# Kernel optimization log

Measured on AMD Instinct MI355X. Metric: run time of the kernel, lower is better.

Reference implementation:

```python
import jax, jax.numpy as jnp
import numpy as np

N, B, I = 64, 32, 1
EMBED, ACT, DETER, STOCH, HIDDEN = 1536, 16, 2048, 512, 1024
EPS = 1e-5


def _ln(x, g, b):
    m = jnp.mean(x, -1, keepdims=True)
    v = jnp.mean((x - m) ** 2, -1, keepdims=True)
    return (x - m) / jnp.sqrt(v + EPS) * g + b


def setup_inputs() -> dict:
    key = jax.random.key(0)
    ks = jax.random.split(key, 24)
    s = 0.02
    d = {
        "embed": jax.random.normal(ks[0], (N, B, EMBED), jnp.float32),
        "action": jax.random.normal(ks[1], (N, B, ACT), jnp.float32),
        "reset": jnp.zeros((N, B), jnp.bool_),
        "h0": jnp.zeros((B * I, DETER), jnp.float32),
        "z0": jnp.zeros((B * I, STOCH), jnp.float32),
        "noises": jax.random.normal(ks[2], (N, B, I, STOCH), jnp.float32),
        # params
        "W_z": jax.random.normal(ks[3], (HIDDEN, STOCH)) * s,
        "b_z": jnp.zeros((HIDDEN,)),
        "W_a": jax.random.normal(ks[4], (HIDDEN, ACT)) * s,
        "ln_in_g": jnp.ones((HIDDEN,)), "ln_in_b": jnp.zeros((HIDDEN,)),
        "gru_Wih": jax.random.normal(ks[5], (3 * DETER, HIDDEN)) * s,
        "gru_Whh": jax.random.normal(ks[6], (3 * DETER, DETER)) * s,
        "gru_bih": jnp.zeros((3 * DETER,)), "gru_bhh": jnp.zeros((3 * DETER,)),
        "W_ph": jax.random.normal(ks[7], (HIDDEN, DETER)) * s,
        "b_ph": jnp.zeros((HIDDEN,)),
        "W_pe": jax.random.normal(ks[8], (HIDDEN, EMBED)) * s,
        "ln_post_g": jnp.ones((HIDDEN,)), "ln_post_b": jnp.zeros((HIDDEN,)),
        "W_post": jax.random.normal(ks[9], (2 * STOCH, HIDDEN)) * s,
        "b_post": jnp.zeros((2 * STOCH,)),
        "W_prh": jax.random.normal(ks[10], (HIDDEN, DETER)) * s,
        "b_prh": jnp.zeros((HIDDEN,)),
        "ln_pr_g": jnp.ones((HIDDEN,)), "ln_pr_b": jnp.zeros((HIDDEN,)),
        "W_pr": jax.random.normal(ks[11], (2 * STOCH, HIDDEN)) * s,
        "b_pr": jnp.zeros((2 * STOCH,)),
    }
    return d


def _core(embed, action, reset, h0, z0, noises,
          W_z, b_z, W_a, ln_in_g, ln_in_b,
          gru_Wih, gru_Whh, gru_bih, gru_bhh,
          W_ph, b_ph, W_pe, ln_post_g, ln_post_b, W_post, b_post,
          W_prh, b_prh, ln_pr_g, ln_pr_b, W_pr, b_pr):
    n, b = embed.shape[:2]
    # expand to (n, b*I, .) ; I == 1
    embeds = embed.reshape(n, b * I, -1)
    actions = action.reshape(n, b * I, -1)
    masks = (~reset).astype(jnp.float32).reshape(n, b * I, 1)
    noise = noises.reshape(n, b * I, -1)

    def step(carry, xs):
        h, z = carry
        e_t, a_t, m_t, n_t = xs
        h = h * m_t
        z = z * m_t
        x = z @ W_z.T + b_z + a_t @ W_a.T
        za = jax.nn.elu(_ln(x, ln_in_g, ln_in_b))
        # torch GRUCell
        gi = za @ gru_Wih.T + gru_bih
        gh = h @ gru_Whh.T + gru_bhh
        gi_r, gi_u, gi_n = jnp.split(gi, 3, -1)
        gh_r, gh_u, gh_n = jnp.split(gh, 3, -1)
        r = jax.nn.sigmoid(gi_r + gh_r)
        u = jax.nn.sigmoid(gi_u + gh_u)
        cand = jnp.tanh(gi_n + r * gh_n)
        h_new = (1.0 - u) * cand + u * h
        x = h_new @ W_ph.T + b_ph + e_t @ W_pe.T
        post_in = jax.nn.elu(_ln(x, ln_post_g, ln_post_b))
        post = post_in @ W_post.T + b_post
        mean, std_raw = jnp.split(post, 2, -1)
        std = jax.nn.softplus(std_raw) + 0.1
        sample = mean + std * n_t
        return (h_new, sample), (post, h_new, sample)

    (h_last, z_last), (posts, states_h, samples) = jax.lax.scan(
        step, (h0, z0), (embeds, actions, masks, noise))

    # batch prior over all h
    x = states_h @ W_prh.T + b_prh
    x = jax.nn.elu(_ln(x, ln_pr_g, ln_pr_b))
    priors = x @ W_pr.T + b_pr
    features = jnp.concatenate([states_h, samples], -1)

    rs = lambda t: t.reshape(n, b, I, -1)
    return rs(priors), rs(posts), rs(samples), rs(features), h_last, z_last


def reference(embed, action, reset, h0, z0, noises,
              W_z, b_z, W_a, ln_in_g, ln_in_b,
              gru_Wih, gru_Whh, gru_bih, gru_bhh,
              W_ph, b_ph, W_pe, ln_post_g, ln_post_b, W_post, b_post,
              W_prh, b_prh, ln_pr_g, ln_pr_b, W_pr, b_pr):
    return _core(embed, action, reset, h0, z0, noises,
                 W_z, b_z, W_a, ln_in_g, ln_in_b,
                 gru_Wih, gru_Whh, gru_bih, gru_bhh,
                 W_ph, b_ph, W_pe, ln_post_g, ln_post_b, W_post, b_post,
                 W_prh, b_prh, ln_pr_g, ln_pr_b, W_pr, b_pr)
```

## Files before the change

kernel.cpp:

```cpp
#include <hip/hip_runtime.h>
#include <hip/hip_bf16.h>
#include <stdint.h>

#define NSTEP 64
#define BATCH 32
#define EMBED_D 1536
#define ACT_D 16
#define DETER 2048
#define STOCH 512
#define HIDDEN 1024
#define FEAT 2560
#define NBLK 256

typedef __attribute__((ext_vector_type(8))) short bf16x8;
typedef __attribute__((ext_vector_type(4))) float f32x4;

#define MFMA16 __builtin_amdgcn_mfma_f32_16x16x32_bf16
#define AGENT __HIP_MEMORY_SCOPE_AGENT

__device__ __forceinline__ float eluf(float x) { return x > 0.f ? x : expf(x) - 1.f; }
__device__ __forceinline__ float sigf(float x) { return 1.f / (1.f + expf(-x)); }
__device__ __forceinline__ unsigned short f2bf(float f) {
    __hip_bfloat16 h = __float2bfloat16(f);
    return __builtin_bit_cast(unsigned short, h);
}
__device__ __forceinline__ float bf2f(unsigned short u) {
    unsigned v = ((unsigned)u) << 16;
    return __builtin_bit_cast(float, v);
}

__device__ __forceinline__ void stc_u32(unsigned* p, unsigned v) {
    __hip_atomic_store(p, v, __ATOMIC_RELAXED, AGENT);
}
__device__ __forceinline__ void stc_u64(unsigned long long* p, unsigned long long v) {
    __hip_atomic_store(p, v, __ATOMIC_RELAXED, AGENT);
}
__device__ __forceinline__ unsigned long long ldc_u64(const unsigned long long* p) {
    return __hip_atomic_load(p, __ATOMIC_RELAXED, AGENT);
}
__device__ __forceinline__ float ldc_f32(const float* p) {
    return __hip_atomic_load(p, __ATOMIC_RELAXED, AGENT);
}
__device__ __forceinline__ int ldc_i32(const int* p) {
    return __hip_atomic_load(p, __ATOMIC_RELAXED, AGENT);
}
__device__ __forceinline__ void stc_i32(int* p, int v) {
    __hip_atomic_store(p, v, __ATOMIC_RELAXED, AGENT);
}
__device__ __forceinline__ bf16x8 ldc_bf8(const unsigned short* p) {
    union { unsigned long long q[2]; bf16x8 v; } u;
    u.q[0] = ldc_u64((const unsigned long long*)p);
    u.q[1] = ldc_u64((const unsigned long long*)(p + 4));
    return u.v;
}
__device__ __forceinline__ ushort4 ldc_us4(const unsigned short* p) {
    unsigned long long q = ldc_u64((const unsigned long long*)p);
    return __builtin_bit_cast(ushort4, q);
}

__device__ __forceinline__ void gbar3(int* flags, int* release, int epoch) {
    asm volatile("s_waitcnt vmcnt(0)" ::: "memory");
    __syncthreads();
    if (blockIdx.x == 0) {
        int tid = threadIdx.x;
        if (tid >= 1 && tid < NBLK) {
            while (ldc_i32(&flags[tid * 32]) < epoch) __builtin_amdgcn_s_sleep(4);
        }
        asm volatile("" ::: "memory");
        __syncthreads();
        if (tid < 32) stc_i32(&release[tid * 32], epoch);
    } else {
        if (threadIdx.x == 0) {
            stc_i32(&flags[blockIdx.x * 32], epoch);
            int* rel = &release[(blockIdx.x & 31) * 32];
            while (ldc_i32(rel) < epoch) __builtin_amdgcn_s_sleep(4);
        }
        asm volatile("" ::: "memory");
        __syncthreads();
    }
}

__global__ __launch_bounds__(256) void k_cvt_all(
    const float* __restrict__ s0, unsigned short* __restrict__ d0,
    const float* __restrict__ s1, unsigned short* __restrict__ d1,
    const float* __restrict__ s2, unsigned short* __restrict__ d2,
    const float* __restrict__ s3, unsigned short* __restrict__ d3,
    const float* __restrict__ s4, unsigned short* __restrict__ d4)
{
    long long e = ((long long)blockIdx.x * 256 + threadIdx.x) * 4;
    const float* src; unsigned short* dst; long long off;
    if (e < 524288)        { src = s0; dst = d0; off = e; }
    else if (e < 6815744)  { src = s1; dst = d1; off = e - 524288; }
    else if (e < 19398656) { src = s2; dst = d2; off = e - 6815744; }
    else if (e < 21495808) { src = s3; dst = d3; off = e - 19398656; }
    else if (e < 22544384) { src = s4; dst = d4; off = e - 21495808; }
    else return;
    float4 v = *reinterpret_cast<const float4*>(src + off);
    ushort4 o;
    o.x = f2bf(v.x); o.y = f2bf(v.y); o.z = f2bf(v.z); o.w = f2bf(v.w);
    *reinterpret_cast<ushort4*>(dst + off) = o;
}

__global__ __launch_bounds__(256) void k_setup(
    const float* __restrict__ h0, const float* __restrict__ z0,
    const uint8_t* __restrict__ reset0,
    float* __restrict__ h0m, unsigned short* __restrict__ h16m0,
    unsigned short* __restrict__ z16m, int* __restrict__ flags)
{
    int gid = blockIdx.x * 256 + threadIdx.x;
    int idx = gid * 4;
    if (idx < BATCH * DETER) {
        int b = idx >> 11;
        float m = reset0[b] ? 0.f : 1.f;
        float4 v = *reinterpret_cast<const float4*>(h0 + idx);
        v.x *= m; v.y *= m; v.z *= m; v.w *= m;
        *reinterpret_cast<float4*>(h0m + idx) = v;
        ushort4 o;
        o.x = f2bf(v.x); o.y = f2bf(v.y); o.z = f2bf(v.z); o.w = f2bf(v.w);
        *reinterpret_cast<ushort4*>(h16m0 + idx) = o;
    } else if (idx < BATCH * DETER + BATCH * STOCH) {
        int zi = idx - BATCH * DETER;
        int b = zi >> 9;
        float m = reset0[b] ? 0.f : 1.f;
        float4 v = *reinterpret_cast<const float4*>(z0 + zi);
        ushort4 o;
        o.x = f2bf(v.x * m); o.y = f2bf(v.y * m); o.z = f2bf(v.z * m); o.w = f2bf(v.w * m);
        *reinterpret_cast<ushort4*>(z16m + zi) = o;
    }
    if (gid < 9216) flags[gid] = 0;
}

__global__ __launch_bounds__(256) void k_preA(
    const float* __restrict__ action, const float* __restrict__ Wa,
    const float* __restrict__ bz, float* __restrict__ preA)
{
    __shared__ float al[16];
    int r = blockIdx.x, t = threadIdx.x;
    if (t < 16) al[t] = action[r * 16 + t];
    __syncthreads();
#pragma unroll
    for (int c = 0; c < 4; ++c) {
        int j = t + c * 256;
        const float* wr = Wa + j * 16;
        float s = bz[j];
#pragma unroll
        for (int k = 0; k < 16; ++k) s += al[k] * wr[k];
        preA[(size_t)r * 1024 + j] = s;
    }
}

__global__ __launch_bounds__(256) void gemm_mfma(
    const float* __restrict__ A, int lda,
    const float* __restrict__ B, int ldb,
    const float* __restrict__ bias,
    float* __restrict__ C, int ldc, int K)
{
    __shared__ unsigned short Alds[64 * 72];
    __shared__ unsigned short Blds[64 * 72];
    int t = threadIdx.x;
    int nb = blockIdx.x, mb = blockIdx.y;
    int w = t >> 6, l = t & 63, l15 = l & 15, kg = l >> 4;
    f32x4 acc[4] = {{0,0,0,0},{0,0,0,0},{0,0,0,0},{0,0,0,0}};
    int srow = t >> 2, skq = (t & 3) * 16;
    const float* Asrc = A + (size_t)(mb * 64 + srow) * lda + skq;
    const float* Bsrc = B + (size_t)(nb * 64 + srow) * ldb + skq;
    unsigned short* Adst = &Alds[srow * 72 + skq];
    unsigned short* Bdst = &Blds[srow * 72 + skq];
    for (int kt = 0; kt < K; kt += 64) {
        __syncthreads();
#pragma unroll
        for (int c = 0; c < 16; c += 4) {
            float4 va = *reinterpret_cast<const float4*>(Asrc + kt + c);
            float4 vb = *reinterpret_cast<const float4*>(Bsrc + kt + c);
            ushort4 oa, ob;
            oa.x = f2bf(va.x); oa.y = f2bf(va.y); oa.z = f2bf(va.z); oa.w = f2bf(va.w);
            ob.x = f2bf(vb.x); ob.y = f2bf(vb.y); ob.z = f2bf(vb.z); ob.w = f2bf(vb.w);
            *reinterpret_cast<ushort4*>(Adst + c) = oa;
            *reinterpret_cast<ushort4*>(Bdst + c) = ob;
        }
        __syncthreads();
#pragma unroll
        for (int ks = 0; ks < 2; ks++) {
            bf16x8 a = *reinterpret_cast<const bf16x8*>(&Alds[(w * 16 + l15) * 72 + ks * 32 + kg * 8]);
#pragma unroll
            for (int nt = 0; nt < 4; nt++) {
                bf16x8 b = *reinterpret_cast<const bf16x8*>(&Blds[(nt * 16 + l15) * 72 + ks * 32 + kg * 8]);
                acc[nt] = MFMA16(a, b, acc[nt], 0, 0, 0);
            }
        }
    }
#pragma unroll
    for (int nt = 0; nt < 4; nt++) {
        int n = nb * 64 + nt * 16 + l15;
        float bv = bias[n];
#pragma unroll
        for (int i = 0; i < 4; i++) {
            C[(size_t)(mb * 64 + w * 16 + kg * 4 + i) * ldc + n] = acc[nt][i] + bv;
        }
    }
}

__global__ __launch_bounds__(256) void ln_elu_rows(
    float* __restrict__ X, const float* __restrict__ g, const float* __restrict__ bb)
{
    __shared__ float sbuf[256], qbuf[256];
    int r = blockIdx.x, t = threadIdx.x;
    float* row = X + (size_t)r * HIDDEN;
    float4 v = reinterpret_cast<const float4*>(row)[t];
    sbuf[t] = (v.x + v.y) + (v.z + v.w);
    qbuf[t] = (v.x * v.x + v.y * v.y) + (v.z * v.z + v.w * v.w);
    __syncthreads();
    for (int off = 128; off > 0; off >>= 1) {
        if (t < off) { sbuf[t] += sbuf[t + off]; qbuf[t] += qbuf[t + off]; }
        __syncthreads();
    }
    float mean = sbuf[0] / HIDDEN;
    float var = qbuf[0] / HIDDEN - mean * mean;
    float rstd = rsqrtf(var + 1e-5f);
    float4 gg = reinterpret_cast<const float4*>(g)[t];
    float4 bv = reinterpret_cast<const float4*>(bb)[t];
    float4 o;
    o.x = eluf((v.x - mean) * rstd * gg.x + bv.x);
    o.y = eluf((v.y - mean) * rstd * gg.y + bv.y);
    o.z = eluf((v.z - mean) * rstd * gg.z + bv.z);
    o.w = eluf((v.w - mean) * rstd * gg.w + bv.w);
    reinterpret_cast<float4*>(row)[t] = o;
}

__global__ __launch_bounds__(256) void k_copy_last(
    const float* __restrict__ feat63, const float* __restrict__ samp63,
    float* __restrict__ hlast, float* __restrict__ zlast)
{
    int i = blockIdx.x * 256 + threadIdx.x;
    if (i < BATCH * DETER) {
        int b = i / DETER, k = i % DETER;
        hlast[i] = feat63[(size_t)b * FEAT + k];
    }
    if (i < BATCH * STOCH) zlast[i] = samp63[i];
}

struct ScanArgs {
    const unsigned short *Wz16, *Wih16, *Whh16, *Wph16, *Wpo16;
    const float *bih, *bhh, *b_post;
    const float *ln_in_g, *ln_in_b, *ln_post_g, *ln_post_b;
    const float *h0m;
    const uint8_t *reset;
    const float *noises;
    float *postsPreA, *priorsPreE, *samples, *feats;
    unsigned short *z16m, *x1b, *x2b, *h16u, *h16m0, *h16m1;
    float *x1parts, *x2parts;
    int *flags, *release;
};

__device__ __forceinline__ void ln_stats2(const float* __restrict__ parts, float* stat,
                                          float* scratch, int tid) {
    int row = tid & 31, grp = tid >> 5;
    float s = 0.f, q = 0.f;
#pragma unroll
    for (int i = 0; i < 4; ++i) {
        union { unsigned long long u; float f[2]; } c;
        c.u = ldc_u64((const unsigned long long*)parts + (size_t)(grp * 4 + i) * 32 + row);
        s += c.f[0]; q += c.f[1];
    }
    scratch[row * 16 + grp] = s;
    scratch[512 + row * 16 + grp] = q;
    __syncthreads();
    if (tid < 32) {
        float ss = 0.f, qq = 0.f;
#pragma unroll
        for (int g = 0; g < 16; ++g) {
            ss += scratch[tid * 16 + g];
            qq += scratch[512 + tid * 16 + g];
        }
        float mean = ss * (1.f / 1024.f);
        float var = qq * (1.f / 1024.f) - mean * mean;
        stat[tid] = mean;
        stat[32 + tid] = rsqrtf(var + 1e-5f);
    }
}

__device__ __forceinline__ void ln_fill512(unsigned short* Asm, const unsigned short* __restrict__ src,
                                           const float* __restrict__ g, const float* __restrict__ bb,
                                           const float* stat, int tid) {
    int row = tid & 31, kb = (tid >> 5) * 64;
    float mean = stat[row], rstd = stat[32 + row];
#pragma unroll 2
    for (int c = 0; c < 8; ++c) {
        int k = kb + c * 8;
        ushort4 u0 = ldc_us4(src + (size_t)row * 1024 + k);
        ushort4 u1 = ldc_us4(src + (size_t)row * 1024 + k + 4);
        float4 g0 = *reinterpret_cast<const float4*>(g + k);
        float4 g1 = *reinterpret_cast<const float4*>(g + k + 4);
        float4 b0 = *reinterpret_cast<const float4*>(bb + k);
        float4 b1 = *reinterpret_cast<const float4*>(bb + k + 4);
        ushort4 o0, o1;
        o0.x = f2bf(eluf((bf2f(u0.x) - mean) * rstd * g0.x + b0.x));
        o0.y = f2bf(eluf((bf2f(u0.y) - mean) * rstd * g0.y + b0.y));
        o0.z = f2bf(eluf((bf2f(u0.z) - mean) * rstd * g0.z + b0.z));
        o0.w = f2bf(eluf((bf2f(u0.w) - mean) * rstd * g0.w + b0.w));
        o1.x = f2bf(eluf((bf2f(u1.x) - mean) * rstd * g1.x + b1.x));
        o1.y = f2bf(eluf((bf2f(u1.y) - mean) * rstd * g1.y + b1.y));
        o1.z = f2bf(eluf((bf2f(u1.z) - mean) * rstd * g1.z + b1.z));
        o1.w = f2bf(eluf((bf2f(u1.w) - mean) * rstd * g1.w + b1.w));
        *reinterpret_cast<ushort4*>(Asm + row * 1032 + k) = o0;
        *reinterpret_cast<ushort4*>(Asm + row * 1032 + k + 4) = o1;
    }
}

__global__ __launch_bounds__(512, 1) void k_scan(ScanArgs a) {
    __shared__ char smem[93184];
    unsigned short* Asm = (unsigned short*)smem;
    float* cbuf  = (float*)(smem + 66048);
    float* stat  = (float*)(smem + 66048 + 8192);
    float* stat2 = (float*)(smem + 90624);
    float* hbuf  = (float*)(smem + 91136);

    const int bid = blockIdx.x;
    const int tid = threadIdx.x;
    const int w = tid >> 6, l = tid & 63, l15 = l & 15, kg = l >> 4;
    int epoch = 0;

    for (int t = 0; t < NSTEP; ++t) {
        const float* preA_t = a.postsPreA + (size_t)t * 32768;
        const float* preE_t = a.priorsPreE + (size_t)t * 32768;
        float* posts_t = a.postsPreA + (size_t)t * 32768;
        float* samples_t = a.samples + (size_t)t * 16384;
        float* feats_t = a.feats + (size_t)t * 81920;
        const float* featsPrev = a.feats + (size_t)(t - 1) * 81920;
        const unsigned short* h16cur = (t & 1) ? a.h16m1 : a.h16m0;
        unsigned short* h16nxt = (t & 1) ? a.h16m0 : a.h16m1;

        if (bid < 64) {
            int j0 = bid * 16;
            if (tid < 256) {
                const unsigned short* A0 = a.z16m + l15 * 512 + w * 128 + kg * 8;
                const unsigned short* A1 = A0 + 16 * 512;
                const unsigned short* Bp = a.Wz16 + (size_t)(j0 + l15) * 512 + w * 128 + kg * 8;
                f32x4 c0 = {0,0,0,0}, c1 = {0,0,0,0};
#pragma unroll
                for (int ks = 0; ks < 4; ++ks) {
                    bf16x8 b = *reinterpret_cast<const bf16x8*>(Bp + ks * 32);
                    c0 = MFMA16(ldc_bf8(A0 + ks * 32), b, c0, 0, 0, 0);
                    c1 = MFMA16(ldc_bf8(A1 + ks * 32), b, c1, 0, 0, 0);
                }
#pragma unroll
                for (int i = 0; i < 4; ++i) {
                    cbuf[w * 512 + (kg * 4 + i) * 16 + l15] = c0[i];
                    cbuf[w * 512 + (16 + kg * 4 + i) * 16 + l15] = c1[i];
                }
            }
            __syncthreads();
            if (tid < 256) {
                int r = tid >> 3, c2 = (tid & 7) * 2;
                int base = r * 16 + c2;
                float v0 = cbuf[base] + cbuf[512 + base] + cbuf[1024 + base] + cbuf[1536 + base]
                         + preA_t[r * 1024 + j0 + c2];
                float v1 = cbuf[base + 1] + cbuf[512 + base + 1] + cbuf[1024 + base + 1] + cbuf[1536 + base + 1]
                         + preA_t[r * 1024 + j0 + c2 + 1];
                unsigned short u0 = f2bf(v0), u1 = f2bf(v1);
                stc_u32((unsigned*)(a.x1b + (size_t)r * 1024 + j0 + c2),
                        (unsigned)u0 | ((unsigned)u1 << 16));
                float w0 = bf2f(u0), w1 = bf2f(u1);
                float s = w0 + w1, q = w0 * w0 + w1 * w1;
                s += __shfl_xor(s, 1); q += __shfl_xor(q, 1);
                s += __shfl_xor(s, 2); q += __shfl_xor(q, 2);
                s += __shfl_xor(s, 4); q += __shfl_xor(q, 4);
                if ((tid & 7) == 0) {
                    union { float f[2]; unsigned long long u; } pu;
                    pu.f[0] = s; pu.f[1] = q;
                    stc_u64((unsigned long long*)(a.x1parts + ((size_t)bid * 32 + r) * 2), pu.u);
                }
            }
        }
        epoch++; gbar3(a.flags, a.release, epoch);

        if (bid < 128) {
            int j0 = bid * 16;
            ln_stats2(a.x1parts, stat2, cbuf, tid);
            __syncthreads();
            ln_fill512(Asm, a.x1b, a.ln_in_g, a.ln_in_b, stat2, tid);
            __syncthreads();
            f32x4 cr = {0,0,0,0}, cu = {0,0,0,0}, cn = {0,0,0,0};
            if (w < 4) {
                int rowgrp = w & 1, kh = w >> 1;
                const unsigned short* ap = Asm + (rowgrp * 16 + l15) * 1032 + kh * 512 + kg * 8;
                const unsigned short* br = a.Wih16 + (size_t)(j0 + l15) * 1024 + kh * 512 + kg * 8;
                const unsigned short* bu = br + (size_t)2048 * 1024;
                const unsigned short* bn = bu + (size_t)2048 * 1024;
#pragma unroll 4
                for (int ks = 0; ks < 16; ++ks) {
                    bf16x8 av = *reinterpret_cast<const bf16x8*>(ap + ks * 32);
                    cr = MFMA16(av, *reinterpret_cast<const bf16x8*>(br + ks * 32), cr, 0, 0, 0);
                    cu = MFMA16(av, *reinterpret_cast<const bf16x8*>(bu + ks * 32), cu, 0, 0, 0);
                    cn = MFMA16(av, *reinterpret_cast<const bf16x8*>(bn + ks * 32), cn, 0, 0, 0);
                }
            } else {
                int idx = w - 4, rowgrp = idx & 1, kh = idx >> 1;
                const unsigned short* hp = h16cur + (size_t)(rowgrp * 16 + l15) * 2048 + kh * 1024 + kg * 8;
                const unsigned short* br = a.Whh16 + (size_t)(j0 + l15) * 2048 + kh * 1024 + kg * 8;
                const unsigned short* bu = br + (size_t)2048 * 2048;
                const unsigned short* bn = bu + (size_t)2048 * 2048;
#pragma unroll 4
                for (int ks = 0; ks < 32; ++ks) {
                    bf16x8 av = ldc_bf8(hp + ks * 32);
                    cr = MFMA16(av, *reinterpret_cast<const bf16x8*>(br + ks * 32), cr, 0, 0, 0);
                    cu = MFMA16(av, *reinterpret_cast<const bf16x8*>(bu + ks * 32), cu, 0, 0, 0);
                    cn = MFMA16(av, *reinterpret_cast<const bf16x8*>(bn + ks * 32), cn, 0, 0, 0);
                }
            }
#pragma unroll
            for (int i = 0; i < 4; ++i) {
                int o = (kg * 4 + i) * 16 + l15;
                cbuf[w * 768 + 0 * 256 + o] = cr[i];
                cbuf[w * 768 + 1 * 256 + o] = cu[i];
                cbuf[w * 768 + 2 * 256 + o] = cn[i];
            }
            __syncthreads();
            {
                int row = tid >> 4, col = tid & 15;
                int rowgrp = row >> 4, rr = row & 15;
                int o = rr * 16 + col;
                int j = j0 + col;
                float gr = cbuf[rowgrp * 768 + 0 * 256 + o] + cbuf[(2 + rowgrp) * 768 + 0 * 256 + o] + a.bih[j];
                float gu = cbuf[rowgrp * 768 + 1 * 256 + o] + cbuf[(2 + rowgrp) * 768 + 1 * 256 + o] + a.bih[j + 2048];
                float gn = cbuf[rowgrp * 768 + 2 * 256 + o] + cbuf[(2 + rowgrp) * 768 + 2 * 256 + o] + a.bih[j + 4096];
                float hr = cbuf[(4 + rowgrp) * 768 + 0 * 256 + o] + cbuf[(6 + rowgrp) * 768 + 0 * 256 + o] + a.bhh[j];
                float hu = cbuf[(4 + rowgrp) * 768 + 1 * 256 + o] + cbuf[(6 + rowgrp) * 768 + 1 * 256 + o] + a.bhh[j + 2048];
                float hn = cbuf[(4 + rowgrp) * 768 + 2 * 256 + o] + cbuf[(6 + rowgrp) * 768 + 2 * 256 + o] + a.bhh[j + 4096];
                float r_ = sigf(gr + hr), u_ = sigf(gu + hu);
                float cand = tanhf(gn + r_ * hn);
                float m = a.reset[t * 32 + row] ? 0.f : 1.f;
                float hpv = (t == 0) ? a.h0m[(size_t)row * 2048 + j]
                                     : ldc_f32(featsPrev + (size_t)row * 2560 + j);
                hbuf[row * 16 + col] = (1.f - u_) * cand + u_ * (m * hpv);
            }
            __syncthreads();
            if (tid < 256) {
                int b = tid >> 3, c2 = (tid & 7) * 2;
                float h0v = hbuf[b * 16 + c2], h1v = hbuf[b * 16 + c2 + 1];
                int j = j0 + c2;
                union { float f[2]; unsigned long long u; } fu;
                fu.f[0] = h0v; fu.f[1] = h1v;
                stc_u64((unsigned long long*)(feats_t + (size_t)b * 2560 + j), fu.u);
                unsigned short g0 = f2bf(h0v), g1 = f2bf(h1v);
                stc_u32((unsigned*)(a.h16u + (size_t)b * 2048 + j),
                        (unsigned)g0 | ((unsigned)g1 << 16));
                float mn = (t < 63) ? (a.reset[(t + 1) * 32 + b] ? 0.f : 1.f) : 1.f;
                unsigned short n0 = f2bf(h0v * mn), n1 = f2bf(h1v * mn);
                stc_u32((unsigned*)(h16nxt + (size_t)b * 2048 + j),
                        (unsigned)n0 | ((unsigned)n1 << 16));
            }
        }
        epoch++; gbar3(a.flags, a.release, epoch);

        if (bid < 64) {
            int j0 = bid * 16;
            {
                int rowgrp = w & 1, kq = w >> 1;
                const unsigned short* Ap = a.h16u + (size_t)(rowgrp * 16 + l15) * 2048 + kq * 512 + kg * 8;
                const unsigned short* Bp = a.Wph16 + (size_t)(j0 + l15) * 2048 + kq * 512 + kg * 8;
                f32x4 c0 = {0,0,0,0};
#pragma unroll 4
                for (int ks = 0; ks < 16; ++ks) {
                    c0 = MFMA16(ldc_bf8(Ap + ks * 32),
                                *reinterpret_cast<const bf16x8*>(Bp + ks * 32), c0, 0, 0, 0);
                }
#pragma unroll
                for (int i = 0; i < 4; ++i)
                    cbuf[w * 256 + (kg * 4 + i) * 16 + l15] = c0[i];
            }
            __syncthreads();
            if (tid < 256) {
                int r = tid >> 3, c2 = (tid & 7) * 2;
                int rowgrp2 = r >> 4, rr = r & 15;
                float v0 = 0.f, v1 = 0.f;
#pragma unroll
                for (int kq2 = 0; kq2 < 4; ++kq2) {
                    v0 += cbuf[(kq2 * 2 + rowgrp2) * 256 + rr * 16 + c2];
                    v1 += cbuf[(kq2 * 2 + rowgrp2) * 256 + rr * 16 + c2 + 1];
                }
                v0 += preE_t[(size_t)r * 1024 + j0 + c2];
                v1 += preE_t[(size_t)r * 1024 + j0 + c2 + 1];
                unsigned short u0 = f2bf(v0), u1 = f2bf(v1);
                stc_u32((unsigned*)(a.x2b + (size_t)r * 1024 + j0 + c2),
                        (unsigned)u0 | ((unsigned)u1 << 16));
                float w0 = bf2f(u0), w1 = bf2f(u1);
                float s = w0 + w1, q = w0 * w0 + w1 * w1;
                s += __shfl_xor(s, 1); q += __shfl_xor(q, 1);
                s += __shfl_xor(s, 2); q += __shfl_xor(q, 2);
                s += __shfl_xor(s, 4); q += __shfl_xor(q, 4);
                if ((tid & 7) == 0) {
                    union { float f[2]; unsigned long long u; } pu;
                    pu.f[0] = s; pu.f[1] = q;
                    stc_u64((unsigned long long*)(a.x2parts + ((size_t)bid * 32 + r) * 2), pu.u);
                }
            }
        }
        epoch++; gbar3(a.flags, a.release, epoch);

        if (bid < 32) {
            int j0 = bid * 16;
            ln_stats2(a.x2parts, stat, cbuf, tid);
            __syncthreads();
            ln_fill512(Asm, a.x2b, a.ln_post_g, a.ln_post_b, stat, tid);
            __syncthreads();
            {
                int tile = w >> 2, mt = (w >> 1) & 1, kh = w & 1;
                const unsigned short* ap = Asm + (mt * 16 + l15) * 1032 + kh * 512 + kg * 8;
                int n = tile ? (512 + j0 + l15) : (j0 + l15);
                const unsigned short* Bp = a.Wpo16 + (size_t)n * 1024 + kh * 512 + kg * 8;
                f32x4 c = {0,0,0,0};
#pragma unroll 4
                for (int ks = 0; ks < 16; ++ks) {
                    c = MFMA16(*reinterpret_cast<const bf16x8*>(ap + ks * 32),
                               *reinterpret_cast<const bf16x8*>(Bp + ks * 32), c, 0, 0, 0);
                }
#pragma unroll
                for (int i = 0; i < 4; ++i)
                    cbuf[w * 256 + (kg * 4 + i) * 16 + l15] = c[i];
            }
            __syncthreads();
            if (tid < 256) {
                int b = tid >> 3, c2 = (tid & 7) * 2;
                int j = j0 + c2;
                int mt2 = b >> 4, rr = b & 15, o = rr * 16;
                float pm0 = cbuf[(mt2 * 2 + 0) * 256 + o + c2] + cbuf[(mt2 * 2 + 1) * 256 + o + c2] + a.b_post[j];
                float pm1 = cbuf[(mt2 * 2 + 0) * 256 + o + c2 + 1] + cbuf[(mt2 * 2 + 1) * 256 + o + c2 + 1] + a.b_post[j + 1];
                float ps0 = cbuf[(4 + mt2 * 2 + 0) * 256 + o + c2] + cbuf[(4 + mt2 * 2 + 1) * 256 + o + c2] + a.b_post[512 + j];
                float ps1 = cbuf[(4 + mt2 * 2 + 0) * 256 + o + c2 + 1] + cbuf[(4 + mt2 * 2 + 1) * 256 + o + c2 + 1] + a.b_post[512 + j + 1];
                posts_t[(size_t)b * 1024 + j] = pm0;
                posts_t[(size_t)b * 1024 + j + 1] = pm1;
                posts_t[(size_t)b * 1024 + 512 + j] = ps0;
                posts_t[(size_t)b * 1024 + 512 + j + 1] = ps1;
                float sp0 = fmaxf(ps0, 0.f) + log1pf(expf(-fabsf(ps0)));
                float sp1 = fmaxf(ps1, 0.f) + log1pf(expf(-fabsf(ps1)));
                float n0v = a.noises[(size_t)t * 16384 + b * 512 + j];
                float n1v = a.noises[(size_t)t * 16384 + b * 512 + j + 1];
                float smp0 = pm0 + (sp0 + 0.1f) * n0v;
                float smp1 = pm1 + (sp1 + 0.1f) * n1v;
                samples_t[(size_t)b * 512 + j] = smp0;
                samples_t[(size_t)b * 512 + j + 1] = smp1;
                feats_t[(size_t)b * 2560 + 2048 + j] = smp0;
                feats_t[(size_t)b * 2560 + 2048 + j + 1] = smp1;
                float mn = (t < 63) ? (a.reset[(t + 1) * 32 + b] ? 0.f : 1.f) : 1.f;
                unsigned short z0_ = f2bf(smp0 * mn), z1_ = f2bf(smp1 * mn);
                stc_u32((unsigned*)(a.z16m + (size_t)b * 512 + j),
                        (unsigned)z0_ | ((unsigned)z1_ << 16));
            }
        }
        epoch++; gbar3(a.flags, a.release, epoch);
    }
}

#define WS_WZ16   ((size_t)0)
#define WS_WIH16  ((size_t)1048576)
#define WS_WHH16  ((size_t)13631488)
#define WS_WPH16  ((size_t)38797312)
#define WS_WPO16  ((size_t)42991616)
#define WS_Z16M   ((size_t)45088768)
#define WS_H16M0  ((size_t)45121536)
#define WS_H16M1  ((size_t)45252608)
#define WS_H16U   ((size_t)45383680)
#define WS_H0M    ((size_t)45514752)
#define WS_X1B    ((size_t)45776896)
#define WS_X2B    ((size_t)45842432)
#define WS_X1P    ((size_t)45907968)
#define WS_X2P    ((size_t)45924352)
#define WS_FLAGS  ((size_t)45940736)
#define WS_REL    ((size_t)45973504)
#define WS_PRX    WS_WIH16

extern "C" void kernel_launch(void* const* d_in, const int* in_sizes, int n_in,
                              void* d_out, int out_size, void* d_ws, size_t ws_size,
                              hipStream_t stream)
{
    (void)in_sizes; (void)n_in; (void)out_size; (void)ws_size;
    const float*   embed  = (const float*)d_in[0];
    const float*   action = (const float*)d_in[1];
    const uint8_t* reset  = (const uint8_t*)d_in[2];
    const float*   h0     = (const float*)d_in[3];
    const float*   z0     = (const float*)d_in[4];
    const float*   noises = (const float*)d_in[5];
    const float*   W_z    = (const float*)d_in[6];
    const float*   b_z    = (const float*)d_in[7];
    const float*   W_a    = (const float*)d_in[8];
    const float*   ln_in_g = (const float*)d_in[9];
    const float*   ln_in_b = (const float*)d_in[10];
    const float*   Wih    = (const float*)d_in[11];
    const float*   Whh    = (const float*)d_in[12];
    const float*   bih    = (const float*)d_in[13];
    const float*   bhh    = (const float*)d_in[14];
    const float*   W_ph   = (const float*)d_in[15];
    const float*   b_ph   = (const float*)d_in[16];
    const float*   W_pe   = (const float*)d_in[17];
    const float*   ln_post_g = (const float*)d_in[18];
    const float*   ln_post_b = (const float*)d_in[19];
    const float*   W_post = (const float*)d_in[20];
    const float*   b_post = (const float*)d_in[21];
    const float*   W_prh  = (const float*)d_in[22];
    const float*   b_prh  = (const float*)d_in[23];
    const float*   ln_pr_g = (const float*)d_in[24];
    const float*   ln_pr_b = (const float*)d_in[25];
    const float*   W_pr   = (const float*)d_in[26];
    const float*   b_pr   = (const float*)d_in[27];

    float* out     = (float*)d_out;
    float* priors  = out;
    float* posts   = out + 2097152;
    float* samples = out + 4194304;
    float* feats   = out + 5242880;
    float* hlast   = out + 10485760;
    float* zlast   = out + 10551296;

    char* ws = (char*)d_ws;
    unsigned short* Wz16  = (unsigned short*)(ws + WS_WZ16);
    unsigned short* Wih16 = (unsigned short*)(ws + WS_WIH16);
    unsigned short* Whh16 = (unsigned short*)(ws + WS_WHH16);
    unsigned short* Wph16 = (unsigned short*)(ws + WS_WPH16);
    unsigned short* Wpo16 = (unsigned short*)(ws + WS_WPO16);
    unsigned short* z16m  = (unsigned short*)(ws + WS_Z16M);
    unsigned short* h16m0 = (unsigned short*)(ws + WS_H16M0);
    unsigned short* h16m1 = (unsigned short*)(ws + WS_H16M1);
    unsigned short* h16u  = (unsigned short*)(ws + WS_H16U);
    float*          h0m   = (float*)(ws + WS_H0M);
    unsigned short* x1b   = (unsigned short*)(ws + WS_X1B);
    unsigned short* x2b   = (unsigned short*)(ws + WS_X2B);
    float*          x1p   = (float*)(ws + WS_X1P);
    float*          x2p   = (float*)(ws + WS_X2P);
    int*            flags = (int*)(ws + WS_FLAGS);
    int*            release = (int*)(ws + WS_REL);
    float*          prx   = (float*)(ws + WS_PRX);

    dim3 blk(256);

    k_cvt_all<<<dim3(22016), blk, 0, stream>>>(W_z, Wz16, Wih, Wih16, Whh, Whh16,
                                               W_ph, Wph16, W_post, Wpo16);
    k_setup<<<dim3(80), blk, 0, stream>>>(h0, z0, reset, h0m, h16m0, z16m, flags);

    k_preA<<<dim3(2048), blk, 0, stream>>>(action, W_a, b_z, posts);
    gemm_mfma<<<dim3(16, 32), blk, 0, stream>>>(embed, EMBED_D, W_pe, EMBED_D, b_ph,
                                                priors, HIDDEN, EMBED_D);

    ScanArgs sa;
    sa.Wz16 = Wz16; sa.Wih16 = Wih16; sa.Whh16 = Whh16; sa.Wph16 = Wph16; sa.Wpo16 = Wpo16;
    sa.bih = bih; sa.bhh = bhh; sa.b_post = b_post;
    sa.ln_in_g = ln_in_g; sa.ln_in_b = ln_in_b; sa.ln_post_g = ln_post_g; sa.ln_post_b = ln_post_b;
    sa.h0m = h0m; sa.reset = reset; sa.noises = noises;
    sa.postsPreA = posts; sa.priorsPreE = priors; sa.samples = samples; sa.feats = feats;
    sa.z16m = z16m; sa.x1b = x1b; sa.x2b = x2b; sa.h16u = h16u;
    sa.h16m0 = h16m0; sa.h16m1 = h16m1;
    sa.x1parts = x1p; sa.x2parts = x2p;
    sa.flags = flags; sa.release = release;

    k_scan<<<dim3(NBLK), dim3(512), 0, stream>>>(sa);

    gemm_mfma<<<dim3(16, 32), blk, 0, stream>>>(feats, FEAT, W_prh, DETER, b_prh,
                                                prx, HIDDEN, DETER);
    ln_elu_rows<<<dim3(2048), blk, 0, stream>>>(prx, ln_pr_g, ln_pr_b);
    gemm_mfma<<<dim3(16, 32), blk, 0, stream>>>(prx, HIDDEN, W_pr, HIDDEN, b_pr,
                                                priors, HIDDEN, HIDDEN);

    k_copy_last<<<dim3(256), blk, 0, stream>>>(
        feats + (size_t)(NSTEP - 1) * BATCH * FEAT,
        samples + (size_t)(NSTEP - 1) * BATCH * STOCH,
        hlast, zlast);
}
```

Before: 4.353 ms.

## Double scan block size to 1024 threads and split K across more waves

The persistent scan kernel now launches 1024 threads per block instead of 512. The GRU, prior-hidden and posterior MFMA loops split the reduction dimension over twice as many waves, and the partial results are summed through a larger shared-memory buffer. Each wave runs a shorter serial MFMA chain, which is meant to cut the latency of every sequential step. In exchange the blocks use more LDS and registers, reduce more partials, and extra threads sit idle in the LN phases.

```diff
diff --git a/kernel.cpp b/kernel.cpp
--- a/kernel.cpp
+++ b/kernel.cpp
@@ -254,16 +254,18 @@
 
 __device__ __forceinline__ void ln_stats2(const float* __restrict__ parts, float* stat,
                                           float* scratch, int tid) {
-    int row = tid & 31, grp = tid >> 5;
-    float s = 0.f, q = 0.f;
-#pragma unroll
-    for (int i = 0; i < 4; ++i) {
-        union { unsigned long long u; float f[2]; } c;
-        c.u = ldc_u64((const unsigned long long*)parts + (size_t)(grp * 4 + i) * 32 + row);
-        s += c.f[0]; q += c.f[1];
-    }
-    scratch[row * 16 + grp] = s;
-    scratch[512 + row * 16 + grp] = q;
+    if (tid < 512) {
+        int row = tid & 31, grp = tid >> 5;
+        float s = 0.f, q = 0.f;
+#pragma unroll
+        for (int i = 0; i < 4; ++i) {
+            union { unsigned long long u; float f[2]; } c;
+            c.u = ldc_u64((const unsigned long long*)parts + (size_t)(grp * 4 + i) * 32 + row);
+            s += c.f[0]; q += c.f[1];
+        }
+        scratch[row * 16 + grp] = s;
+        scratch[512 + row * 16 + grp] = q;
+    }
     __syncthreads();
     if (tid < 32) {
         float ss = 0.f, qq = 0.f;
@@ -282,6 +284,7 @@
 __device__ __forceinline__ void ln_fill512(unsigned short* Asm, const unsigned short* __restrict__ src,
                                            const float* __restrict__ g, const float* __restrict__ bb,
                                            const float* stat, int tid) {
+    if (tid >= 512) return;
     int row = tid & 31, kb = (tid >> 5) * 64;
     float mean = stat[row], rstd = stat[32 + row];
 #pragma unroll 2
@@ -307,13 +310,13 @@
     }
 }
 
-__global__ __launch_bounds__(512, 1) void k_scan(ScanArgs a) {
-    __shared__ char smem[93184];
+__global__ __launch_bounds__(1024, 1) void k_scan(ScanArgs a) {
+    __shared__ char smem[118272];
     unsigned short* Asm = (unsigned short*)smem;
     float* cbuf  = (float*)(smem + 66048);
-    float* stat  = (float*)(smem + 66048 + 8192);
-    float* stat2 = (float*)(smem + 90624);
-    float* hbuf  = (float*)(smem + 91136);
+    float* stat  = (float*)(smem + 115200);
+    float* stat2 = (float*)(smem + 115712);
+    float* hbuf  = (float*)(smem + 116224);
 
     const int bid = blockIdx.x;
     const int tid = threadIdx.x;
@@ -381,27 +384,27 @@
             ln_fill512(Asm, a.x1b, a.ln_in_g, a.ln_in_b, stat2, tid);
             __syncthreads();
             f32x4 cr = {0,0,0,0}, cu = {0,0,0,0}, cn = {0,0,0,0};
-            if (w < 4) {
-                int rowgrp = w & 1, kh = w >> 1;
-                const unsigned short* ap = Asm + (rowgrp * 16 + l15) * 1032 + kh * 512 + kg * 8;
-                const unsigned short* br = a.Wih16 + (size_t)(j0 + l15) * 1024 + kh * 512 + kg * 8;
+            if (w < 8) {
+                int rowgrp = w & 1, kq = w >> 1;
+                const unsigned short* ap = Asm + (rowgrp * 16 + l15) * 1032 + kq * 256 + kg * 8;
+                const unsigned short* br = a.Wih16 + (size_t)(j0 + l15) * 1024 + kq * 256 + kg * 8;
                 const unsigned short* bu = br + (size_t)2048 * 1024;
                 const unsigned short* bn = bu + (size_t)2048 * 1024;
 #pragma unroll 4
-                for (int ks = 0; ks < 16; ++ks) {
+                for (int ks = 0; ks < 8; ++ks) {
                     bf16x8 av = *reinterpret_cast<const bf16x8*>(ap + ks * 32);
                     cr = MFMA16(av, *reinterpret_cast<const bf16x8*>(br + ks * 32), cr, 0, 0, 0);
                     cu = MFMA16(av, *reinterpret_cast<const bf16x8*>(bu + ks * 32), cu, 0, 0, 0);
                     cn = MFMA16(av, *reinterpret_cast<const bf16x8*>(bn + ks * 32), cn, 0, 0, 0);
                 }
             } else {
-                int idx = w - 4, rowgrp = idx & 1, kh = idx >> 1;
-                const unsigned short* hp = h16cur + (size_t)(rowgrp * 16 + l15) * 2048 + kh * 1024 + kg * 8;
-                const unsigned short* br = a.Whh16 + (size_t)(j0 + l15) * 2048 + kh * 1024 + kg * 8;
+                int idx = w - 8, rowgrp = idx & 1, kq = idx >> 1;
+                const unsigned short* hp = h16cur + (size_t)(rowgrp * 16 + l15) * 2048 + kq * 512 + kg * 8;
+                const unsigned short* br = a.Whh16 + (size_t)(j0 + l15) * 2048 + kq * 512 + kg * 8;
                 const unsigned short* bu = br + (size_t)2048 * 2048;
                 const unsigned short* bn = bu + (size_t)2048 * 2048;
 #pragma unroll 4
-                for (int ks = 0; ks < 32; ++ks) {
+                for (int ks = 0; ks < 16; ++ks) {
                     bf16x8 av = ldc_bf8(hp + ks * 32);
                     cr = MFMA16(av, *reinterpret_cast<const bf16x8*>(br + ks * 32), cr, 0, 0, 0);
                     cu = MFMA16(av, *reinterpret_cast<const bf16x8*>(bu + ks * 32), cu, 0, 0, 0);
@@ -416,17 +419,25 @@
                 cbuf[w * 768 + 2 * 256 + o] = cn[i];
             }
             __syncthreads();
-            {
+            if (tid < 512) {
                 int row = tid >> 4, col = tid & 15;
                 int rowgrp = row >> 4, rr = row & 15;
                 int o = rr * 16 + col;
                 int j = j0 + col;
-                float gr = cbuf[rowgrp * 768 + 0 * 256 + o] + cbuf[(2 + rowgrp) * 768 + 0 * 256 + o] + a.bih[j];
-                float gu = cbuf[rowgrp * 768 + 1 * 256 + o] + cbuf[(2 + rowgrp) * 768 + 1 * 256 + o] + a.bih[j + 2048];
-                float gn = cbuf[rowgrp * 768 + 2 * 256 + o] + cbuf[(2 + rowgrp) * 768 + 2 * 256 + o] + a.bih[j + 4096];
-                float hr = cbuf[(4 + rowgrp) * 768 + 0 * 256 + o] + cbuf[(6 + rowgrp) * 768 + 0 * 256 + o] + a.bhh[j];
-                float hu = cbuf[(4 + rowgrp) * 768 + 1 * 256 + o] + cbuf[(6 + rowgrp) * 768 + 1 * 256 + o] + a.bhh[j + 2048];
-                float hn = cbuf[(4 + rowgrp) * 768 + 2 * 256 + o] + cbuf[(6 + rowgrp) * 768 + 2 * 256 + o] + a.bhh[j + 4096];
+                float gr = 0.f, gu = 0.f, gn = 0.f, hr = 0.f, hu = 0.f, hn = 0.f;
+#pragma unroll
+                for (int kq = 0; kq < 4; ++kq) {
+                    int wi = kq * 2 + rowgrp;
+                    gr += cbuf[wi * 768 + 0 * 256 + o];
+                    gu += cbuf[wi * 768 + 1 * 256 + o];
+                    gn += cbuf[wi * 768 + 2 * 256 + o];
+                    int wh = 8 + kq * 2 + rowgrp;
+                    hr += cbuf[wh * 768 + 0 * 256 + o];
+                    hu += cbuf[wh * 768 + 1 * 256 + o];
+                    hn += cbuf[wh * 768 + 2 * 256 + o];
+                }
+                gr += a.bih[j]; gu += a.bih[j + 2048]; gn += a.bih[j + 4096];
+                hr += a.bhh[j]; hu += a.bhh[j + 2048]; hn += a.bhh[j + 4096];
                 float r_ = sigf(gr + hr), u_ = sigf(gu + hu);
                 float cand = tanhf(gn + r_ * hn);
                 float m = a.reset[t * 32 + row] ? 0.f : 1.f;
@@ -456,12 +467,12 @@
         if (bid < 64) {
             int j0 = bid * 16;
             {
-                int rowgrp = w & 1, kq = w >> 1;
-                const unsigned short* Ap = a.h16u + (size_t)(rowgrp * 16 + l15) * 2048 + kq * 512 + kg * 8;
-                const unsigned short* Bp = a.Wph16 + (size_t)(j0 + l15) * 2048 + kq * 512 + kg * 8;
+                int rowgrp = w & 1, k8 = w >> 1;
+                const unsigned short* Ap = a.h16u + (size_t)(rowgrp * 16 + l15) * 2048 + k8 * 256 + kg * 8;
+                const unsigned short* Bp = a.Wph16 + (size_t)(j0 + l15) * 2048 + k8 * 256 + kg * 8;
                 f32x4 c0 = {0,0,0,0};
 #pragma unroll 4
-                for (int ks = 0; ks < 16; ++ks) {
+                for (int ks = 0; ks < 8; ++ks) {
                     c0 = MFMA16(ldc_bf8(Ap + ks * 32),
                                 *reinterpret_cast<const bf16x8*>(Bp + ks * 32), c0, 0, 0, 0);
                 }
@@ -475,9 +486,9 @@
                 int rowgrp2 = r >> 4, rr = r & 15;
                 float v0 = 0.f, v1 = 0.f;
 #pragma unroll
-                for (int kq2 = 0; kq2 < 4; ++kq2) {
-                    v0 += cbuf[(kq2 * 2 + rowgrp2) * 256 + rr * 16 + c2];
-                    v1 += cbuf[(kq2 * 2 + rowgrp2) * 256 + rr * 16 + c2 + 1];
+                for (int k8 = 0; k8 < 8; ++k8) {
+                    v0 += cbuf[(k8 * 2 + rowgrp2) * 256 + rr * 16 + c2];
+                    v1 += cbuf[(k8 * 2 + rowgrp2) * 256 + rr * 16 + c2 + 1];
                 }
                 v0 += preE_t[(size_t)r * 1024 + j0 + c2];
                 v1 += preE_t[(size_t)r * 1024 + j0 + c2 + 1];
@@ -505,13 +516,13 @@
             ln_fill512(Asm, a.x2b, a.ln_post_g, a.ln_post_b, stat, tid);
             __syncthreads();
             {
-                int tile = w >> 2, mt = (w >> 1) & 1, kh = w & 1;
-                const unsigned short* ap = Asm + (mt * 16 + l15) * 1032 + kh * 512 + kg * 8;
+                int tile = w >> 3, mt = (w >> 2) & 1, kq = w & 3;
+                const unsigned short* ap = Asm + (mt * 16 + l15) * 1032 + kq * 256 + kg * 8;
                 int n = tile ? (512 + j0 + l15) : (j0 + l15);
-                const unsigned short* Bp = a.Wpo16 + (size_t)n * 1024 + kh * 512 + kg * 8;
+                const unsigned short* Bp = a.Wpo16 + (size_t)n * 1024 + kq * 256 + kg * 8;
                 f32x4 c = {0,0,0,0};
 #pragma unroll 4
-                for (int ks = 0; ks < 16; ++ks) {
+                for (int ks = 0; ks < 8; ++ks) {
                     c = MFMA16(*reinterpret_cast<const bf16x8*>(ap + ks * 32),
                                *reinterpret_cast<const bf16x8*>(Bp + ks * 32), c, 0, 0, 0);
                 }
@@ -524,10 +535,16 @@
                 int b = tid >> 3, c2 = (tid & 7) * 2;
                 int j = j0 + c2;
                 int mt2 = b >> 4, rr = b & 15, o = rr * 16;
-                float pm0 = cbuf[(mt2 * 2 + 0) * 256 + o + c2] + cbuf[(mt2 * 2 + 1) * 256 + o + c2] + a.b_post[j];
-                float pm1 = cbuf[(mt2 * 2 + 0) * 256 + o + c2 + 1] + cbuf[(mt2 * 2 + 1) * 256 + o + c2 + 1] + a.b_post[j + 1];
-                float ps0 = cbuf[(4 + mt2 * 2 + 0) * 256 + o + c2] + cbuf[(4 + mt2 * 2 + 1) * 256 + o + c2] + a.b_post[512 + j];
-                float ps1 = cbuf[(4 + mt2 * 2 + 0) * 256 + o + c2 + 1] + cbuf[(4 + mt2 * 2 + 1) * 256 + o + c2 + 1] + a.b_post[512 + j + 1];
+                float pm0 = 0.f, pm1 = 0.f, ps0 = 0.f, ps1 = 0.f;
+#pragma unroll
+                for (int kq = 0; kq < 4; ++kq) {
+                    pm0 += cbuf[(mt2 * 4 + kq) * 256 + o + c2];
+                    pm1 += cbuf[(mt2 * 4 + kq) * 256 + o + c2 + 1];
+                    ps0 += cbuf[(8 + mt2 * 4 + kq) * 256 + o + c2];
+                    ps1 += cbuf[(8 + mt2 * 4 + kq) * 256 + o + c2 + 1];
+                }
+                pm0 += a.b_post[j]; pm1 += a.b_post[j + 1];
+                ps0 += a.b_post[512 + j]; ps1 += a.b_post[512 + j + 1];
                 posts_t[(size_t)b * 1024 + j] = pm0;
                 posts_t[(size_t)b * 1024 + j + 1] = pm1;
                 posts_t[(size_t)b * 1024 + 512 + j] = ps0;
@@ -652,7 +669,7 @@
     sa.x1parts = x1p; sa.x2parts = x2p;
     sa.flags = flags; sa.release = release;
 
-    k_scan<<<dim3(NBLK), dim3(512), 0, stream>>>(sa);
+    k_scan<<<dim3(NBLK), dim3(1024), 0, stream>>>(sa);
 
     gemm_mfma<<<dim3(16, 32), blk, 0, stream>>>(feats, FEAT, W_prh, DETER, b_prh,
                                                 prx, HIDDEN, DETER);
```

New measurement: 5.102 ms. 1.17x slower.
